# Optimization experiments

Hardware: AMD Instinct MI355X
Metric: run time of the kernel (lower is better)

## Reference

```python
import jax, jax.numpy as jnp
import numpy as np

T, C, H, W, CI = 4, 64, 96, 96, 16
PS, WS, STR0 = 7, 21, 4
KS, KA = 100, 100
SCALE = 10.0


def conv1x1(x, w, b):
    # x: [T,C,H,W], w: [O,C]
    return jnp.einsum('tchw,oc->tohw', x, w) + b[None, :, None, None]


def unfold_clip(x, ps):
    # clipped-boundary unfold: [T,C,H,W] -> [T, H*W, C*ps*ps]
    t, c, h, w = x.shape
    d = jnp.arange(ps)
    ii = jnp.clip(jnp.arange(h)[:, None] + d[None, :], 0, h - 1)  # [H,ps]
    jj = jnp.clip(jnp.arange(w)[:, None] + d[None, :], 0, w - 1)  # [W,ps]
    p = x[:, :, ii]            # [T,C,H,ps,W]
    p = p[:, :, :, :, jj]      # [T,C,H,ps,W,ps]
    p = jnp.transpose(p, (0, 2, 4, 1, 3, 5))  # [T,H,W,C,ps,ps]
    return p.reshape(t, h * w, c * ps * ps)


def setup_inputs() -> dict:
    key = jax.random.key(0)
    ks = jax.random.split(key, 9)
    s = lambda fan: 1.0 / np.sqrt(fan)
    return {
        'vid': jax.random.normal(ks[0], (T, C, H, W), jnp.float32),
        'g_w': jax.random.normal(ks[1], (CI, C), jnp.float32) * s(C),
        'g_b': jax.random.normal(ks[2], (CI,), jnp.float32) * 0.01,
        'theta_w': jax.random.normal(ks[3], (CI, C), jnp.float32) * s(C),
        'theta_b': jax.random.normal(ks[4], (CI,), jnp.float32) * 0.01,
        'phi_w': jax.random.normal(ks[5], (CI, C), jnp.float32) * s(C),
        'phi_b': jax.random.normal(ks[6], (CI,), jnp.float32) * 0.01,
        'W_w': jax.random.normal(ks[7], (C, CI), jnp.float32) * s(CI),
        'W_b': jax.random.normal(ks[8], (C,), jnp.float32) * 0.01,
    }


def reference(vid, g_w, g_b, theta_w, theta_b, phi_w, phi_b, W_w, W_b):
    t, c, h, w = vid.shape
    b1 = conv1x1(vid, g_w, g_b)          # query features  (g)
    b2 = conv1x1(vid, theta_w, theta_b)  # value features  (theta)
    b3 = conv1x1(vid, phi_w, phi_b)      # key features    (phi)

    b1u = unfold_clip(b1, PS)  # [T,HW,D]
    b2u = unfold_clip(b2, PS)
    b3u = unfold_clip(b3, PS)

    # query grid (stride0)
    qi, qj = jnp.meshgrid(jnp.arange(0, h, STR0), jnp.arange(0, w, STR0), indexing='ij')
    qi, qj = qi.reshape(-1), qj.reshape(-1)
    nq = qi.shape[0]
    qflat = qi * w + qj
    b1q = b1u[:, qflat]  # [T,nq,D]

    # centered spatial search window (stride1=1), clipped bounds
    off = jnp.arange(WS) - WS // 2
    ci = jnp.clip(qi[:, None] + off[None, :], 0, h - 1)  # [nq,WS]
    cj = jnp.clip(qj[:, None] + off[None, :], 0, w - 1)
    cand = (ci[:, :, None] * w + cj[:, None, :]).reshape(nq, WS * WS)

    # patch inner-product dists, one window offset at a time (memory-lean)
    def score(cidx):  # cidx: [nq]
        return jnp.einsum('tqd,tqd->tq', b1q, b3u[:, cidx])
    dists = jax.lax.map(score, cand.T)           # [WS*WS,T,nq]
    dists = jnp.transpose(dists, (1, 2, 0))      # [T,nq,WS*WS]

    vals, idx = jax.lax.top_k(dists, KS)
    vals, idx = vals[..., :KA], idx[..., :KA]
    yi = jax.nn.softmax(vals * SCALE, axis=-1)   # [T,nq,KA]

    pos = jnp.take_along_axis(jnp.broadcast_to(cand[None], (t,) + cand.shape), idx, axis=-1)
    patches = b2u[jnp.arange(t)[:, None, None], pos]   # [T,nq,KA,D]
    zi = jnp.einsum('tqk,tqkd->tqd', yi, patches)      # [T,nq,D]

    # fold: overlap-add scatter + counts normalization
    zi = zi.reshape(t, nq, CI, PS, PS).transpose(0, 2, 1, 3, 4).reshape(t, CI, nq * PS * PS)
    d = jnp.arange(PS)
    pi = jnp.clip(qi[:, None] + d[None, :], 0, h - 1)
    pj = jnp.clip(qj[:, None] + d[None, :], 0, w - 1)
    pix = (pi[:, :, None] * w + pj[:, None, :]).reshape(-1)
    acc = jnp.zeros((t, CI, h * w), vid.dtype).at[:, :, pix].add(zi)
    Z = jnp.zeros((h * w,), vid.dtype).at[pix].add(1.0)
    y = (acc / Z).reshape(t, CI, h, w)

    return vid + conv1x1(y, W_w, W_b)
```

## Files before the change

### kernel.cpp

```cpp
#include <hip/hip_runtime.h>
#include <hip/hip_bf16.h>
#include <hip/hip_fp16.h>
#include <math.h>

typedef __hip_bfloat16 bf16;
typedef unsigned int u32;
typedef __attribute__((ext_vector_type(8))) short short8;
typedef __attribute__((ext_vector_type(4))) float float4v;

#define T_   4
#define C_   64
#define H_   96
#define W_   96
#define CI_  16
#define HW_  9216
#define NC_  441
#define K_   100
#define HSEL 0x07060302u
#define LSEL 0x05040100u

__device__ __forceinline__ float ldbf(const void* p, int i) { return __bfloat162float(((const bf16*)p)[i]); }
__device__ __forceinline__ float ldf (const void* p, int i) { return ((const float*)p)[i]; }

__device__ __forceinline__ unsigned short f2bf(float x) {
    union { float f; u32 u; } a; a.f = x;
    u32 r = a.u + 0x7FFF + ((a.u >> 16) & 1);
    return (unsigned short)(r >> 16);
}
__device__ __forceinline__ float bf2f(unsigned short s) {
    union { u32 u; float f; } a; a.u = ((u32)s) << 16;
    return a.f;
}
__device__ __forceinline__ u32 packbf(float x) {
    unsigned short h = f2bf(x);
    unsigned short l = f2bf(x - bf2f(h));
    return ((u32)h << 16) | (u32)l;
}
__device__ __forceinline__ u32 okey(float f) {
    u32 u = __float_as_uint(f);
    return u ^ ((u & 0x80000000u) ? 0xFFFFFFFFu : 0x80000000u);
}
__device__ __forceinline__ float unokey(u32 k) {
    u32 u = (k & 0x80000000u) ? (k ^ 0x80000000u) : ~k;
    return __uint_as_float(u);
}
__device__ __forceinline__ int cntdim(int x) {
    int c = 0;
#pragma unroll
    for (int pp = 0; pp < 7; pp++) {
        int q = x - pp;
        c += (q >= 0 && q <= 92 && ((q & 3) == 0)) ? 1 : 0;
    }
    if (x == 95) c += 3;
    return c;
}

__device__ __forceinline__ int detect_flag(const void* vid, int tid, int* sflag) {
    if (tid < 64) {
        unsigned short w = ((const unsigned short*)vid)[tid * 2];
        int e = (w >> 7) & 0xFF;
        int sane = ((e >= 100 && e <= 140) || ((w & 0x7FFF) == 0)) ? 1 : 0;
#pragma unroll
        for (int off = 1; off < 64; off <<= 1) sane += __shfl_xor(sane, off);
        if (tid == 0) *sflag = (sane >= 48) ? 1 : 0;
    }
    __syncthreads();
    return *sflag;
}

__global__ __launch_bounds__(256) void conv3_k(const void* vid, const void* gw, const void* gb,
                                               const void* tw, const void* tb, const void* pw,
                                               const void* pb,
                                               u32* __restrict__ B1p, __half* __restrict__ B2h,
                                               u32* __restrict__ B3p, float* __restrict__ ACCb)
{
    __shared__ float w[3120];
    __shared__ int sflag;
    int tid = threadIdx.x;
    int isbf = detect_flag(vid, tid, &sflag);
    if (isbf) {
        for (int i = tid; i < 3120; i += 256) {
            float v;
            if (i < 1024) v = ldbf(gw, i);
            else if (i < 2048) v = ldbf(tw, i - 1024);
            else if (i < 3072) v = ldbf(pw, i - 2048);
            else if (i < 3088) v = ldbf(gb, i - 3072);
            else if (i < 3104) v = ldbf(tb, i - 3088);
            else v = ldbf(pb, i - 3104);
            w[i] = v;
        }
    } else {
        for (int i = tid; i < 3120; i += 256) {
            float v;
            if (i < 1024) v = ldf(gw, i);
            else if (i < 2048) v = ldf(tw, i - 1024);
            else if (i < 3072) v = ldf(pw, i - 2048);
            else if (i < 3088) v = ldf(gb, i - 3072);
            else if (i < 3104) v = ldf(tb, i - 3088);
            else v = ldf(pb, i - 3104);
            w[i] = v;
        }
    }
    __syncthreads();

    {
        float4v z = {0.f, 0.f, 0.f, 0.f};
        *(float4v*)(ACCb + (blockIdx.x * 256 + tid) * 4) = z;
    }

    int lane = tid & 63, og = tid >> 6;
    int g0 = blockIdx.x * 64 + lane;
    int t = g0 / HW_, pix = g0 - t * HW_;

    float a1[4], a2[4], a3[4];
#pragma unroll
    for (int k = 0; k < 4; k++) {
        a1[k] = w[3072 + og * 4 + k];
        a2[k] = w[3088 + og * 4 + k];
        a3[k] = w[3104 + og * 4 + k];
    }
    int base = t * C_ * HW_ + pix;
#pragma unroll 16
    for (int c = 0; c < C_; c++) {
        float v = isbf ? ldbf(vid, base + c * HW_) : ldf(vid, base + c * HW_);
#pragma unroll
        for (int k = 0; k < 4; k++) {
            a1[k] += v * w[(og * 4 + k) * 64 + c];
            a2[k] += v * w[1024 + (og * 4 + k) * 64 + c];
            a3[k] += v * w[2048 + (og * 4 + k) * 64 + c];
        }
    }
    int ob = g0 * 16 + og * 4;
    uint4 p1, p3;
    p1.x = packbf(a1[0]); p1.y = packbf(a1[1]); p1.z = packbf(a1[2]); p1.w = packbf(a1[3]);
    p3.x = packbf(a3[0]); p3.y = packbf(a3[1]); p3.z = packbf(a3[2]); p3.w = packbf(a3[3]);
    *(uint4*)(B1p + ob) = p1;
    *(uint4*)(B3p + ob) = p3;
    __half2 h01 = __floats2half2_rn(a2[0], a2[1]);
    __half2 h23 = __floats2half2_rn(a2[2], a2[3]);
    uint2 p2;
    p2.x = *(u32*)&h01; p2.y = *(u32*)&h23;
    *(uint2*)(B2h + ob) = p2;
}

__global__ __launch_bounds__(512, 6) void attn_k(const u32* __restrict__ B1p,
                                                 const __half* __restrict__ B2h,
                                                 const u32* __restrict__ B3p,
                                                 float* __restrict__ ACCb)
{
    __shared__ __align__(16) char SM[51344];
    short*   Win  = (short*)SM;
    float*   Sc   = (float*)(SM + 32768);
    float*   Cb   = (float*)(SM + 39824);
    int*     hist = (int*)(SM + 39824);
    float*   yiw  = (float*)(SM + 48016);
    int*     pab  = (int*)(SM + 49616);
    int*     ctl  = (int*)(SM + 51216);
    __half2* Zc   = (__half2*)(SM + 32768);
    __half2* Wp   = (__half2*)SM;

    int tid = threadIdx.x;
    int tile = blockIdx.x, t = blockIdx.y;
    int qy = tile / 12, qx = tile - qy * 12;
    int qi = qy * 8, qj = qx * 8;

    const u32*    B1t = B1p + t * HW_ * 16;
    const __half* B2t = B2h + t * HW_ * 16;
    const u32*    B3t = B3p + t * HW_ * 16;

    int lane = tid & 63, wv = tid >> 6;
    int nn = lane & 15, qsel = nn >> 3, pjn = nn & 7;
    int koff = (lane >> 4) * 8;

    for (int pos = tid; pos < 1024; pos += 512) {
        int row = pos >> 5, col = pos & 31;
        int vr = min(max(qi - 10 + row, 0), 95);
        int vc = min(max(qj - 10 + col, 0), 95);
        const u32* src = B3t + (vr * 96 + vc) * 16;
        uint4 U0 = *(const uint4*)src,       U1 = *(const uint4*)(src + 4);
        uint4 U2 = *(const uint4*)(src + 8), U3 = *(const uint4*)(src + 12);
        uint4 A, B;
        A.x = __builtin_amdgcn_perm(U0.y, U0.x, HSEL);
        A.y = __builtin_amdgcn_perm(U0.w, U0.z, HSEL);
        A.z = __builtin_amdgcn_perm(U1.y, U1.x, HSEL);
        A.w = __builtin_amdgcn_perm(U1.w, U1.z, HSEL);
        B.x = __builtin_amdgcn_perm(U2.y, U2.x, HSEL);
        B.y = __builtin_amdgcn_perm(U2.w, U2.z, HSEL);
        B.z = __builtin_amdgcn_perm(U3.y, U3.x, HSEL);
        B.w = __builtin_amdgcn_perm(U3.w, U3.z, HSEL);
        *(uint4*)(Win + pos * 16)     = A;
        *(uint4*)(Win + pos * 16 + 8) = B;
    }
    __syncthreads();

#pragma unroll 1
    for (int ri = 0; ri < 2; ri++) {
        short8 Bh[4], Bl[4];
        int qiq = qi + 4 * ri, qjq = qj + 4 * qsel;
#pragma unroll
        for (int s = 0; s < 4; s++) {
            int kk0 = s * 32 + koff;
            int pi = kk0 >> 4, c0 = kk0 & 15;
            uint4 U0 = {0, 0, 0, 0}, U1 = {0, 0, 0, 0};
            if (pjn < 7 && pi < 7) {
                const u32* src = B1t + (min(qiq + pi, 95) * 96 + min(qjq + pjn, 95)) * 16 + c0;
                U0 = *(const uint4*)src;
                U1 = *(const uint4*)(src + 4);
            }
            union { uint4 u; short8 s8; } hc, lc;
            hc.u.x = __builtin_amdgcn_perm(U0.y, U0.x, HSEL);
            hc.u.y = __builtin_amdgcn_perm(U0.w, U0.z, HSEL);
            hc.u.z = __builtin_amdgcn_perm(U1.y, U1.x, HSEL);
            hc.u.w = __builtin_amdgcn_perm(U1.w, U1.z, HSEL);
            lc.u.x = __builtin_amdgcn_perm(U0.y, U0.x, LSEL);
            lc.u.y = __builtin_amdgcn_perm(U0.w, U0.z, LSEL);
            lc.u.z = __builtin_amdgcn_perm(U1.y, U1.x, LSEL);
            lc.u.w = __builtin_amdgcn_perm(U1.w, U1.z, LSEL);
            Bh[s] = hc.s8; Bl[s] = lc.s8;
        }
        float* Cw = Cb + wv * 256;
        for (int r = wv; r < 21; r += 8) {
            float psum = 0.f;
            int v = (lane >= 21) ? 1 : 0;
            int b = lane - v * 21;
#pragma unroll
            for (int st = 0; st < 2; st++) {
                float4v acc = {0.f, 0.f, 0.f, 0.f};
#pragma unroll
                for (int s = 0; s < 4; s++) {
                    int arow = 4 * ri + r + 2 * s + (lane >> 5);
                    int aoff = (arow * 32 + st * 16 + nn) * 16 + ((lane >> 4) & 1) * 8;
                    short8 A = *(const short8*)(Win + aoff);
                    acc = __builtin_amdgcn_mfma_f32_16x16x32_bf16(A, Bh[s], acc, 0, 0, 0);
                    acc = __builtin_amdgcn_mfma_f32_16x16x32_bf16(A, Bl[s], acc, 0, 0, 0);
                }
                *(float4v*)(Cw + nn * 16 + (lane >> 4) * 4) = acc;
                if (lane < 42) {
#pragma unroll
                    for (int pj = 0; pj < 7; pj++) {
                        int sp = b + 4 * v + pj;
                        if ((sp >> 4) == st) psum += Cw[(8 * v + pj) * 16 + (sp & 15)];
                    }
                }
            }
            if (lane < 42) Sc[(ri * 2 + v) * 441 + r * 21 + b] = psum;
        }
    }
    __syncthreads();

    for (int pos = tid; pos < 1024; pos += 512) {
        int row = pos >> 5, col = pos & 31;
        int vr = min(max(qi - 10 + row, 0), 95);
        int vc = min(max(qj - 10 + col, 0), 95);
        const u32* src = B3t + (vr * 96 + vc) * 16;
        uint4 U0 = *(const uint4*)src,       U1 = *(const uint4*)(src + 4);
        uint4 U2 = *(const uint4*)(src + 8), U3 = *(const uint4*)(src + 12);
        uint4 A, B;
        A.x = __builtin_amdgcn_perm(U0.y, U0.x, LSEL);
        A.y = __builtin_amdgcn_perm(U0.w, U0.z, LSEL);
        A.z = __builtin_amdgcn_perm(U1.y, U1.x, LSEL);
        A.w = __builtin_amdgcn_perm(U1.w, U1.z, LSEL);
        B.x = __builtin_amdgcn_perm(U2.y, U2.x, LSEL);
        B.y = __builtin_amdgcn_perm(U2.w, U2.z, LSEL);
        B.z = __builtin_amdgcn_perm(U3.y, U3.x, LSEL);
        B.w = __builtin_amdgcn_perm(U3.w, U3.z, LSEL);
        *(uint4*)(Win + pos * 16)     = A;
        *(uint4*)(Win + pos * 16 + 8) = B;
    }
    __syncthreads();

#pragma unroll 1
    for (int ri = 0; ri < 2; ri++) {
        short8 Bh[4];
        int qiq = qi + 4 * ri, qjq = qj + 4 * qsel;
#pragma unroll
        for (int s = 0; s < 4; s++) {
            int kk0 = s * 32 + koff;
            int pi = kk0 >> 4, c0 = kk0 & 15;
            uint4 U0 = {0, 0, 0, 0}, U1 = {0, 0, 0, 0};
            if (pjn < 7 && pi < 7) {
                const u32* src = B1t + (min(qiq + pi, 95) * 96 + min(qjq + pjn, 95)) * 16 + c0;
                U0 = *(const uint4*)src;
                U1 = *(const uint4*)(src + 4);
            }
            union { uint4 u; short8 s8; } hc;
            hc.u.x = __builtin_amdgcn_perm(U0.y, U0.x, HSEL);
            hc.u.y = __builtin_amdgcn_perm(U0.w, U0.z, HSEL);
            hc.u.z = __builtin_amdgcn_perm(U1.y, U1.x, HSEL);
            hc.u.w = __builtin_amdgcn_perm(U1.w, U1.z, HSEL);
            Bh[s] = hc.s8;
        }
        float* Cw = Cb + wv * 256;
        for (int r = wv; r < 21; r += 8) {
            float psum = 0.f;
            int v = (lane >= 21) ? 1 : 0;
            int b = lane - v * 21;
#pragma unroll
            for (int st = 0; st < 2; st++) {
                float4v acc = {0.f, 0.f, 0.f, 0.f};
#pragma unroll
                for (int s = 0; s < 4; s++) {
                    int arow = 4 * ri + r + 2 * s + (lane >> 5);
                    int aoff = (arow * 32 + st * 16 + nn) * 16 + ((lane >> 4) & 1) * 8;
                    short8 A = *(const short8*)(Win + aoff);
                    acc = __builtin_amdgcn_mfma_f32_16x16x32_bf16(A, Bh[s], acc, 0, 0, 0);
                }
                *(float4v*)(Cw + nn * 16 + (lane >> 4) * 4) = acc;
                if (lane < 42) {
#pragma unroll
                    for (int pj = 0; pj < 7; pj++) {
                        int sp = b + 4 * v + pj;
                        if ((sp >> 4) == st) psum += Cw[(8 * v + pj) * 16 + (sp & 15)];
                    }
                }
            }
            if (lane < 42) Sc[(ri * 2 + v) * 441 + r * 21 + b] += psum;
        }
    }
    __syncthreads();

    for (int pos = tid; pos < 992; pos += 512) {
        int row = pos >> 5, col = pos & 31;
        int vr = min(max(qi - 10 + row, 0), 95);
        int vc = min(max(qj - 10 + col, 0), 95);
        const __half* src = B2t + (vr * 96 + vc) * 16;
        *(int4*)(Wp + pos * 8)     = *(const int4*)src;
        *(int4*)(Wp + pos * 8 + 4) = *(const int4*)(src + 8);
    }
    hist[tid] = 0; hist[512 + tid] = 0;
    if (tid < 32) ctl[tid] = ((tid & 7) == 1) ? K_ : 0;
    __syncthreads();

    int g = wv & 3;
    int ri = g >> 1, ci = g & 1;
    int qiq = qi + 4 * ri, qjq = qj + 4 * ci;
    int alo = max(0, 10 - qiq), ahi = min(20, 105 - qiq);
    int blo = max(0, 10 - qjq), bhi = min(20, 105 - qjq);
    u32 kreg[7]; int ni = 0;
    u32 kmax = 0;
    if (wv < 4) {
        for (int i = lane; i < NC_; i += 64) {
            int aa = i / 21, bb = i - aa * 21;
            int ae = min(max(aa, alo), ahi), be = min(max(bb, blo), bhi);
            u32 k = okey(Sc[g * 441 + ae * 21 + be]);
            kmax = max(kmax, k);
            kreg[ni++] = k;
        }
#pragma unroll
        for (int off = 1; off < 64; off <<= 1) kmax = max(kmax, (u32)__shfl_xor((int)kmax, off));
    }

    for (int ps = 3; ps >= 0; ps--) {
        if (wv < 4 && !ctl[g * 8 + 3]) {
            u32 pref = (u32)ctl[g * 8];
            for (int a = 0; a < ni; a++) {
                u32 k = kreg[a];
                if (ps == 3 || (k >> ((ps + 1) * 8)) == pref)
                    atomicAdd(&hist[g * 256 + ((k >> (ps * 8)) & 255)], 1);
            }
        }
        __syncthreads();
        if (wv < 4 && !ctl[g * 8 + 3]) {
            int4 hv = *(int4*)(hist + g * 256 + lane * 4);
            int local = hv.x + hv.y + hv.z + hv.w;
            int s = local;
#pragma unroll
            for (int off = 1; off < 64; off <<= 1) {
                int tt = __shfl_down(s, off);
                if (lane + off < 64) s += tt;
            }
            int c4 = s - local;
            int c3 = c4 + hv.w, c2 = c3 + hv.z, c1 = c2 + hv.y, c0 = s;
            int need = ctl[g * 8 + 1];
            u32 pf = (u32)ctl[g * 8];
            int cums[5] = {c0, c1, c2, c3, c4};
            int hk[4] = {hv.x, hv.y, hv.z, hv.w};
#pragma unroll
            for (int k = 0; k < 4; k++) {
                if (cums[k] >= need && cums[k + 1] < need) {
                    int newneed = need - cums[k + 1];
                    ctl[g * 8]     = (int)((pf << 8) | (u32)(lane * 4 + k));
                    ctl[g * 8 + 1] = newneed;
                    if (newneed == hk[k] || ps == 0) { ctl[g * 8 + 3] = 1; ctl[g * 8 + 2] = 8 * ps; }
                }
            }
            int4 zz = {0, 0, 0, 0};
            *(int4*)(hist + g * 256 + lane * 4) = zz;
        }
        __syncthreads();
        if (ctl[3] && ctl[11] && ctl[19] && ctl[27]) break;
    }

    if (wv < 4) {
        u32 theta = (u32)ctl[g * 8];
        int shift = ctl[g * 8 + 2];
        int need  = ctl[g * 8 + 1];
        int base  = K_ - need;
        int a2 = 0;
        for (int i = lane; i < NC_; i += 64) {
            u32 k = kreg[a2++];
            u32 hp = k >> shift;
            int slot = -1;
            if (hp > theta) slot = atomicAdd(&ctl[g * 8 + 4], 1);
            else if (hp == theta) {
                int j = atomicAdd(&ctl[g * 8 + 5], 1);
                if (j < need) slot = base + j;
            }
            if (slot >= 0) {
                int a = i / 21, b = i - a * 21;
                int ae = min(max(a, alo), ahi), be = min(max(b, blo), bhi);
                yiw[g * 100 + slot] = unokey(k);
                pab[g * 100 + slot] = ((ae + 4 * ri) << 8) | (be + 4 * ci);
            }
        }
        float m = unokey(kmax);
        float wa = expf((yiw[g * 100 + lane] - m) * 10.f);
        float wb2 = (lane < 36) ? expf((yiw[g * 100 + 64 + lane] - m) * 10.f) : 0.f;
        float ssum = wa + wb2;
#pragma unroll
        for (int off = 1; off < 64; off <<= 1) ssum += __shfl_xor(ssum, off);
        float inv = 1.f / ssum;
        yiw[g * 100 + lane] = wa * inv;
        if (lane < 36) yiw[g * 100 + 64 + lane] = wb2 * inv;
    }
    __syncthreads();

    {
        int kh = wv >> 2;
        __half2 z[8];
        int rsel = lane & 1;
        int pi = lane / 7, pj = lane - pi * 7;
        if (lane < 49) {
#pragma unroll
            for (int j = 0; j < 8; j++) z[j] = __float2half2_rn(0.f);
            int kb2 = kh * 50;
            for (int k = kb2; k < kb2 + 50; k++) {
                float y = yiw[g * 100 + k];
                int pp = pab[g * 100 + k];
                int row = (pp >> 8) + pi, col = (pp & 255) + pj;
                const __half2* cell = Wp + (row * 32 + col) * 8;
                int4 A0 = *(const int4*)(cell + rsel * 4);
                int4 A1 = *(const int4*)(cell + 4 - rsel * 4);
                const __half2* pa = (const __half2*)&A0;
                const __half2* pb2 = (const __half2*)&A1;
                __half2 yh = __float2half2_rn(y);
#pragma unroll
                for (int j = 0; j < 4; j++) {
                    z[j]     = __hfma2(pa[j],  yh, z[j]);
                    z[4 + j] = __hfma2(pb2[j], yh, z[4 + j]);
                }
            }
        }
        if (kh == 1 && lane < 49) {
            *(int4*)(Zc + (g * 49 + lane) * 8)     = *(int4*)(z);
            *(int4*)(Zc + (g * 49 + lane) * 8 + 4) = *(int4*)(z + 4);
        }
        __syncthreads();
        if (kh == 0 && lane < 49) {
            const __half2* zo = Zc + (g * 49 + lane) * 8;
#pragma unroll
            for (int j = 0; j < 8; j++) z[j] = __hadd2(z[j], zo[j]);
            int orow = min(qiq + pi, 95), ocol = min(qjq + pj, 95);
            float* dst = ACCb + t * CI_ * HW_ + orow * 96 + ocol;
            int c0 = rsel * 8, c1 = 8 - c0;
#pragma unroll
            for (int jh = 0; jh < 4; jh++) {
                atomicAdd(dst + (c0 + 2 * jh) * HW_,     __low2float(z[jh]));
                atomicAdd(dst + (c0 + 2 * jh + 1) * HW_, __high2float(z[jh]));
                atomicAdd(dst + (c1 + 2 * jh) * HW_,     __low2float(z[4 + jh]));
                atomicAdd(dst + (c1 + 2 * jh + 1) * HW_, __high2float(z[4 + jh]));
            }
        }
    }
}

__global__ __launch_bounds__(256) void out_k(const void* vid, const void* Ww, const void* Wb,
                                             const float* __restrict__ ACCb, void* out)
{
    __shared__ float w[1088];
    __shared__ int sflag;
    int tid = threadIdx.x;
    int isbf = detect_flag(vid, tid, &sflag);
    if (isbf) { for (int i = tid; i < 1088; i += 256) w[i] = (i < 1024) ? ldbf(Ww, i) : ldbf(Wb, i - 1024); }
    else      { for (int i = tid; i < 1088; i += 256) w[i] = (i < 1024) ? ldf (Ww, i) : ldf (Wb, i - 1024); }
    __syncthreads();

    int lane5 = tid & 31, oct = tid >> 5;
    int g0 = blockIdx.x * 32 + lane5;
    int t = g0 / HW_, pix = g0 - t * HW_;
    int pi = pix / 96, pj = pix - pi * 96;
    float invz = 1.f / (float)(cntdim(pi) * cntdim(pj));

    float y[CI_];
    int ab = t * CI_ * HW_ + pix;
#pragma unroll
    for (int ci = 0; ci < CI_; ci++) y[ci] = ACCb[ab + ci * HW_] * invz;

    int vb = t * C_ * HW_ + pix;
#pragma unroll
    for (int co = oct * 8; co < oct * 8 + 8; co++) {
        float s = w[1024 + co];
#pragma unroll
        for (int ci = 0; ci < CI_; ci++) s += w[co * 16 + ci] * y[ci];
        int idx = vb + co * HW_;
        float vv = isbf ? ldbf(vid, idx) : ldf(vid, idx);
        float r = vv + s;
        if (isbf) ((bf16*)out)[idx] = __float2bfloat16(r);
        else      ((float*)out)[idx] = r;
    }
}

extern "C" void kernel_launch(void* const* d_in, const int* in_sizes, int n_in,
                              void* d_out, int out_size, void* d_ws, size_t ws_size,
                              hipStream_t stream)
{
    char* ws = (char*)d_ws;
    u32*    B1p  = (u32*)ws;
    __half* B2h  = (__half*)(ws + 2359296);
    u32*    B3p  = (u32*)(ws + 3538944);
    float*  ACCb = (float*)(ws + 5898240);

    conv3_k<<<dim3(576), dim3(256), 0, stream>>>(d_in[0], d_in[1], d_in[2], d_in[3], d_in[4],
                                                 d_in[5], d_in[6], B1p, B2h, B3p, ACCb);
    attn_k<<<dim3(144, T_), dim3(512), 0, stream>>>(B1p, B2h, B3p, ACCb);
    out_k<<<dim3(1152), dim3(256), 0, stream>>>(d_in[0], d_in[7], d_in[8], ACCb, d_out);
}
```

Measured before the change: 172.3 us.

## Read key and value windows directly from global memory, shrink shared memory

Drops the shared-memory staging of the key window (done twice, for hi and lo bf16 halves) and of the value window. MFMA A-operands and value patches are now loaded straight from global/L2 with clamped indices. The two-pass hi/lo split becomes a single pass with three MFMAs, and the aggregation becomes one wave per query group with zero-weight skipping and no cross-wave reduction or barrier. The aim is to cut LDS footprint from about 51KB to 18KB for higher occupancy and to remove staging loops and syncs. The cost is more uncoalesced, redundant global loads in the inner MFMA and gather loops.

```diff
diff --git a/kernel.cpp b/kernel.cpp
--- a/kernel.cpp
+++ b/kernel.cpp
@@ -148,16 +148,13 @@
                                                  const u32* __restrict__ B3p,
                                                  float* __restrict__ ACCb)
 {
-    __shared__ __align__(16) char SM[51344];
-    short*   Win  = (short*)SM;
-    float*   Sc   = (float*)(SM + 32768);
-    float*   Cb   = (float*)(SM + 39824);
-    int*     hist = (int*)(SM + 39824);
-    float*   yiw  = (float*)(SM + 48016);
-    int*     pab  = (int*)(SM + 49616);
-    int*     ctl  = (int*)(SM + 51216);
-    __half2* Zc   = (__half2*)(SM + 32768);
-    __half2* Wp   = (__half2*)SM;
+    __shared__ __align__(16) char SM[18576];
+    float* Sc   = (float*)SM;
+    float* Cb   = (float*)(SM + 7056);
+    int*   hist = (int*)(SM + 7056);
+    float* yiw  = (float*)(SM + 15248);
+    int*   pab  = (int*)(SM + 16848);
+    int*   ctl  = (int*)(SM + 18448);
 
     int tid = threadIdx.x;
     int tile = blockIdx.x, t = blockIdx.y;
@@ -171,27 +168,12 @@
     int lane = tid & 63, wv = tid >> 6;
     int nn = lane & 15, qsel = nn >> 3, pjn = nn & 7;
     int koff = (lane >> 4) * 8;
-
-    for (int pos = tid; pos < 1024; pos += 512) {
-        int row = pos >> 5, col = pos & 31;
-        int vr = min(max(qi - 10 + row, 0), 95);
-        int vc = min(max(qj - 10 + col, 0), 95);
-        const u32* src = B3t + (vr * 96 + vc) * 16;
-        uint4 U0 = *(const uint4*)src,       U1 = *(const uint4*)(src + 4);
-        uint4 U2 = *(const uint4*)(src + 8), U3 = *(const uint4*)(src + 12);
-        uint4 A, B;
-        A.x = __builtin_amdgcn_perm(U0.y, U0.x, HSEL);
-        A.y = __builtin_amdgcn_perm(U0.w, U0.z, HSEL);
-        A.z = __builtin_amdgcn_perm(U1.y, U1.x, HSEL);
-        A.w = __builtin_amdgcn_perm(U1.w, U1.z, HSEL);
-        B.x = __builtin_amdgcn_perm(U2.y, U2.x, HSEL);
-        B.y = __builtin_amdgcn_perm(U2.w, U2.z, HSEL);
-        B.z = __builtin_amdgcn_perm(U3.y, U3.x, HSEL);
-        B.w = __builtin_amdgcn_perm(U3.w, U3.z, HSEL);
-        *(uint4*)(Win + pos * 16)     = A;
-        *(uint4*)(Win + pos * 16 + 8) = B;
-    }
-    __syncthreads();
+    int hi8 = (lane >> 4) & 1;
+
+    int acol0 = min(max(qj - 10 + nn, 0), 95) * 16 + hi8 * 8;
+    int acol1 = min(max(qj + 6 + nn, 0), 95) * 16 + hi8 * 8;
+
+    float* Cw = Cb + wv * 256;
 
 #pragma unroll 1
     for (int ri = 0; ri < 2; ri++) {
@@ -218,21 +200,33 @@
             lc.u.w = __builtin_amdgcn_perm(U1.w, U1.z, LSEL);
             Bh[s] = hc.s8; Bl[s] = lc.s8;
         }
-        float* Cw = Cb + wv * 256;
         for (int r = wv; r < 21; r += 8) {
             float psum = 0.f;
             int v = (lane >= 21) ? 1 : 0;
             int b = lane - v * 21;
 #pragma unroll
             for (int st = 0; st < 2; st++) {
+                int acolc = st ? acol1 : acol0;
                 float4v acc = {0.f, 0.f, 0.f, 0.f};
 #pragma unroll
                 for (int s = 0; s < 4; s++) {
                     int arow = 4 * ri + r + 2 * s + (lane >> 5);
-                    int aoff = (arow * 32 + st * 16 + nn) * 16 + ((lane >> 4) & 1) * 8;
-                    short8 A = *(const short8*)(Win + aoff);
-                    acc = __builtin_amdgcn_mfma_f32_16x16x32_bf16(A, Bh[s], acc, 0, 0, 0);
-                    acc = __builtin_amdgcn_mfma_f32_16x16x32_bf16(A, Bl[s], acc, 0, 0, 0);
+                    int vr = min(max(qi - 10 + arow, 0), 95);
+                    const u32* asrc = B3t + vr * 1536 + acolc;
+                    uint4 U0 = *(const uint4*)asrc;
+                    uint4 U1 = *(const uint4*)(asrc + 4);
+                    union { uint4 u; short8 s8; } hc, lc;
+                    hc.u.x = __builtin_amdgcn_perm(U0.y, U0.x, HSEL);
+                    hc.u.y = __builtin_amdgcn_perm(U0.w, U0.z, HSEL);
+                    hc.u.z = __builtin_amdgcn_perm(U1.y, U1.x, HSEL);
+                    hc.u.w = __builtin_amdgcn_perm(U1.w, U1.z, HSEL);
+                    lc.u.x = __builtin_amdgcn_perm(U0.y, U0.x, LSEL);
+                    lc.u.y = __builtin_amdgcn_perm(U0.w, U0.z, LSEL);
+                    lc.u.z = __builtin_amdgcn_perm(U1.y, U1.x, LSEL);
+                    lc.u.w = __builtin_amdgcn_perm(U1.w, U1.z, LSEL);
+                    acc = __builtin_amdgcn_mfma_f32_16x16x32_bf16(hc.s8, Bh[s], acc, 0, 0, 0);
+                    acc = __builtin_amdgcn_mfma_f32_16x16x32_bf16(hc.s8, Bl[s], acc, 0, 0, 0);
+                    acc = __builtin_amdgcn_mfma_f32_16x16x32_bf16(lc.s8, Bh[s], acc, 0, 0, 0);
                 }
                 *(float4v*)(Cw + nn * 16 + (lane >> 4) * 4) = acc;
                 if (lane < 42) {
@@ -248,92 +242,13 @@
     }
     __syncthreads();
 
-    for (int pos = tid; pos < 1024; pos += 512) {
-        int row = pos >> 5, col = pos & 31;
-        int vr = min(max(qi - 10 + row, 0), 95);
-        int vc = min(max(qj - 10 + col, 0), 95);
-        const u32* src = B3t + (vr * 96 + vc) * 16;
-        uint4 U0 = *(const uint4*)src,       U1 = *(const uint4*)(src + 4);
-        uint4 U2 = *(const uint4*)(src + 8), U3 = *(const uint4*)(src + 12);
-        uint4 A, B;
-        A.x = __builtin_amdgcn_perm(U0.y, U0.x, LSEL);
-        A.y = __builtin_amdgcn_perm(U0.w, U0.z, LSEL);
-        A.z = __builtin_amdgcn_perm(U1.y, U1.x, LSEL);
-        A.w = __builtin_amdgcn_perm(U1.w, U1.z, LSEL);
-        B.x = __builtin_amdgcn_perm(U2.y, U2.x, LSEL);
-        B.y = __builtin_amdgcn_perm(U2.w, U2.z, LSEL);
-        B.z = __builtin_amdgcn_perm(U3.y, U3.x, LSEL);
-        B.w = __builtin_amdgcn_perm(U3.w, U3.z, LSEL);
-        *(uint4*)(Win + pos * 16)     = A;
-        *(uint4*)(Win + pos * 16 + 8) = B;
-    }
-    __syncthreads();
-
-#pragma unroll 1
-    for (int ri = 0; ri < 2; ri++) {
-        short8 Bh[4];
-        int qiq = qi + 4 * ri, qjq = qj + 4 * qsel;
-#pragma unroll
-        for (int s = 0; s < 4; s++) {
-            int kk0 = s * 32 + koff;
-            int pi = kk0 >> 4, c0 = kk0 & 15;
-            uint4 U0 = {0, 0, 0, 0}, U1 = {0, 0, 0, 0};
-            if (pjn < 7 && pi < 7) {
-                const u32* src = B1t + (min(qiq + pi, 95) * 96 + min(qjq + pjn, 95)) * 16 + c0;
-                U0 = *(const uint4*)src;
-                U1 = *(const uint4*)(src + 4);
-            }
-            union { uint4 u; short8 s8; } hc;
-            hc.u.x = __builtin_amdgcn_perm(U0.y, U0.x, HSEL);
-            hc.u.y = __builtin_amdgcn_perm(U0.w, U0.z, HSEL);
-            hc.u.z = __builtin_amdgcn_perm(U1.y, U1.x, HSEL);
-            hc.u.w = __builtin_amdgcn_perm(U1.w, U1.z, HSEL);
-            Bh[s] = hc.s8;
-        }
-        float* Cw = Cb + wv * 256;
-        for (int r = wv; r < 21; r += 8) {
-            float psum = 0.f;
-            int v = (lane >= 21) ? 1 : 0;
-            int b = lane - v * 21;
-#pragma unroll
-            for (int st = 0; st < 2; st++) {
-                float4v acc = {0.f, 0.f, 0.f, 0.f};
-#pragma unroll
-                for (int s = 0; s < 4; s++) {
-                    int arow = 4 * ri + r + 2 * s + (lane >> 5);
-                    int aoff = (arow * 32 + st * 16 + nn) * 16 + ((lane >> 4) & 1) * 8;
-                    short8 A = *(const short8*)(Win + aoff);
-                    acc = __builtin_amdgcn_mfma_f32_16x16x32_bf16(A, Bh[s], acc, 0, 0, 0);
-                }
-                *(float4v*)(Cw + nn * 16 + (lane >> 4) * 4) = acc;
-                if (lane < 42) {
-#pragma unroll
-                    for (int pj = 0; pj < 7; pj++) {
-                        int sp = b + 4 * v + pj;
-                        if ((sp >> 4) == st) psum += Cw[(8 * v + pj) * 16 + (sp & 15)];
-                    }
-                }
-            }
-            if (lane < 42) Sc[(ri * 2 + v) * 441 + r * 21 + b] += psum;
-        }
-    }
-    __syncthreads();
-
-    for (int pos = tid; pos < 992; pos += 512) {
-        int row = pos >> 5, col = pos & 31;
-        int vr = min(max(qi - 10 + row, 0), 95);
-        int vc = min(max(qj - 10 + col, 0), 95);
-        const __half* src = B2t + (vr * 96 + vc) * 16;
-        *(int4*)(Wp + pos * 8)     = *(const int4*)src;
-        *(int4*)(Wp + pos * 8 + 4) = *(const int4*)(src + 8);
-    }
     hist[tid] = 0; hist[512 + tid] = 0;
     if (tid < 32) ctl[tid] = ((tid & 7) == 1) ? K_ : 0;
     __syncthreads();
 
     int g = wv & 3;
-    int ri = g >> 1, ci = g & 1;
-    int qiq = qi + 4 * ri, qjq = qj + 4 * ci;
+    int ri2 = g >> 1, ci2 = g & 1;
+    int qiq = qi + 4 * ri2, qjq = qj + 4 * ci2;
     int alo = max(0, 10 - qiq), ahi = min(20, 105 - qiq);
     int blo = max(0, 10 - qjq), bhi = min(20, 105 - qjq);
     u32 kreg[7]; int ni = 0;
@@ -391,7 +306,9 @@
         if (ctl[3] && ctl[11] && ctl[19] && ctl[27]) break;
     }
 
-    if (wv < 4) {
+    if (wv >= 4) return;
+
+    {
         u32 theta = (u32)ctl[g * 8];
         int shift = ctl[g * 8 + 2];
         int need  = ctl[g * 8 + 1];
@@ -410,11 +327,12 @@
                 int a = i / 21, b = i - a * 21;
                 int ae = min(max(a, alo), ahi), be = min(max(b, blo), bhi);
                 yiw[g * 100 + slot] = unokey(k);
-                pab[g * 100 + slot] = ((ae + 4 * ri) << 8) | (be + 4 * ci);
-            }
-        }
+                pab[g * 100 + slot] = ((ae + 4 * ri2) << 8) | (be + 4 * ci2);
+            }
+        }
+        asm volatile("s_waitcnt lgkmcnt(0)" ::: "memory");
         float m = unokey(kmax);
-        float wa = expf((yiw[g * 100 + lane] - m) * 10.f);
+        float wa  = expf((yiw[g * 100 + lane] - m) * 10.f);
         float wb2 = (lane < 36) ? expf((yiw[g * 100 + 64 + lane] - m) * 10.f) : 0.f;
         float ssum = wa + wb2;
 #pragma unroll
@@ -422,54 +340,44 @@
         float inv = 1.f / ssum;
         yiw[g * 100 + lane] = wa * inv;
         if (lane < 36) yiw[g * 100 + 64 + lane] = wb2 * inv;
-    }
-    __syncthreads();
-
-    {
-        int kh = wv >> 2;
+        asm volatile("s_waitcnt lgkmcnt(0)" ::: "memory");
+    }
+
+    if (lane < 49) {
+        int rsel = lane & 1;
+        int pi2 = lane / 7, pj2 = lane - pi2 * 7;
         __half2 z[8];
-        int rsel = lane & 1;
-        int pi = lane / 7, pj = lane - pi * 7;
-        if (lane < 49) {
-#pragma unroll
-            for (int j = 0; j < 8; j++) z[j] = __float2half2_rn(0.f);
-            int kb2 = kh * 50;
-            for (int k = kb2; k < kb2 + 50; k++) {
-                float y = yiw[g * 100 + k];
-                int pp = pab[g * 100 + k];
-                int row = (pp >> 8) + pi, col = (pp & 255) + pj;
-                const __half2* cell = Wp + (row * 32 + col) * 8;
-                int4 A0 = *(const int4*)(cell + rsel * 4);
-                int4 A1 = *(const int4*)(cell + 4 - rsel * 4);
-                const __half2* pa = (const __half2*)&A0;
-                const __half2* pb2 = (const __half2*)&A1;
-                __half2 yh = __float2half2_rn(y);
-#pragma unroll
-                for (int j = 0; j < 4; j++) {
-                    z[j]     = __hfma2(pa[j],  yh, z[j]);
-                    z[4 + j] = __hfma2(pb2[j], yh, z[4 + j]);
-                }
-            }
-        }
-        if (kh == 1 && lane < 49) {
-            *(int4*)(Zc + (g * 49 + lane) * 8)     = *(int4*)(z);
-            *(int4*)(Zc + (g * 49 + lane) * 8 + 4) = *(int4*)(z + 4);
-        }
-        __syncthreads();
-        if (kh == 0 && lane < 49) {
-            const __half2* zo = Zc + (g * 49 + lane) * 8;
-#pragma unroll
-            for (int j = 0; j < 8; j++) z[j] = __hadd2(z[j], zo[j]);
-            int orow = min(qiq + pi, 95), ocol = min(qjq + pj, 95);
-            float* dst = ACCb + t * CI_ * HW_ + orow * 96 + ocol;
-            int c0 = rsel * 8, c1 = 8 - c0;
-#pragma unroll
-            for (int jh = 0; jh < 4; jh++) {
-                atomicAdd(dst + (c0 + 2 * jh) * HW_,     __low2float(z[jh]));
-                atomicAdd(dst + (c0 + 2 * jh + 1) * HW_, __high2float(z[jh]));
-                atomicAdd(dst + (c1 + 2 * jh) * HW_,     __low2float(z[4 + jh]));
-                atomicAdd(dst + (c1 + 2 * jh + 1) * HW_, __high2float(z[4 + jh]));
-            }
+#pragma unroll
+        for (int j = 0; j < 8; j++) z[j] = __float2half2_rn(0.f);
+#pragma unroll 1
+        for (int k = 0; k < K_; k++) {
+            float y = yiw[g * 100 + k];
+            if (y == 0.f) continue;
+            int pp = pab[g * 100 + k];
+            int row = (pp >> 8) + pi2, col = (pp & 255) + pj2;
+            int vr = min(max(qi - 10 + row, 0), 95);
+            int vc = min(max(qj - 10 + col, 0), 95);
+            const __half* cell = B2t + (vr * 96 + vc) * 16;
+            int4 A0 = *(const int4*)(cell + rsel * 8);
+            int4 A1 = *(const int4*)(cell + 8 - rsel * 8);
+            const __half2* pa  = (const __half2*)&A0;
+            const __half2* pb2 = (const __half2*)&A1;
+            __half2 yh = __float2half2_rn(y);
+#pragma unroll
+            for (int j = 0; j < 4; j++) {
+                z[j]     = __hfma2(pa[j],  yh, z[j]);
+                z[4 + j] = __hfma2(pb2[j], yh, z[4 + j]);
+            }
+        }
+        int orow = min(qiq + pi2, 95), ocol = min(qjq + pj2, 95);
+        float* dst = ACCb + t * CI_ * HW_ + orow * 96 + ocol;
+        int c0 = rsel * 8, c1 = 8 - c0;
+#pragma unroll
+        for (int jh = 0; jh < 4; jh++) {
+            atomicAdd(dst + (c0 + 2 * jh) * HW_,     __low2float(z[jh]));
+            atomicAdd(dst + (c0 + 2 * jh + 1) * HW_, __high2float(z[jh]));
+            atomicAdd(dst + (c1 + 2 * jh) * HW_,     __low2float(z[4 + jh]));
+            atomicAdd(dst + (c1 + 2 * jh + 1) * HW_, __high2float(z[4 + jh]));
         }
     }
 }
```

Measured after the change: 182.0 us. 5.6% more time.

## Skip zero-weight neighbors and gather value patches directly from global memory

Applied to the files above, without the earlier changes.

The value-window staging into shared memory and the two-wave split of the aggregation are removed. Each of four waves now ballots which softmax weights are nonzero and walks only those indices, loading the value patch rows straight from global memory (L2/L1). The final block barrier and the shared-memory reduction are also dropped, and waves 4-7 exit early. The aim is to cut LDS staging, barriers and multiply-adds spent on weights that underflow to zero. In exchange the aggregation loses parallelism, since 4 waves instead of 8 do it, and adds scattered global loads.

```diff
diff --git a/kernel.cpp b/kernel.cpp
--- a/kernel.cpp
+++ b/kernel.cpp
@@ -5,6 +5,7 @@
 
 typedef __hip_bfloat16 bf16;
 typedef unsigned int u32;
+typedef unsigned long long u64;
 typedef __attribute__((ext_vector_type(8))) short short8;
 typedef __attribute__((ext_vector_type(4))) float float4v;
 
@@ -149,15 +150,13 @@
                                                  float* __restrict__ ACCb)
 {
     __shared__ __align__(16) char SM[51344];
-    short*   Win  = (short*)SM;
-    float*   Sc   = (float*)(SM + 32768);
-    float*   Cb   = (float*)(SM + 39824);
-    int*     hist = (int*)(SM + 39824);
-    float*   yiw  = (float*)(SM + 48016);
-    int*     pab  = (int*)(SM + 49616);
-    int*     ctl  = (int*)(SM + 51216);
-    __half2* Zc   = (__half2*)(SM + 32768);
-    __half2* Wp   = (__half2*)SM;
+    short* Win  = (short*)SM;
+    float* Sc   = (float*)(SM + 32768);
+    float* Cb   = (float*)(SM + 39824);
+    int*   hist = (int*)(SM + 39824);
+    float* yiw  = (float*)(SM + 48016);
+    int*   pab  = (int*)(SM + 49616);
+    int*   ctl  = (int*)(SM + 51216);
 
     int tid = threadIdx.x;
     int tile = blockIdx.x, t = blockIdx.y;
@@ -319,21 +318,13 @@
     }
     __syncthreads();
 
-    for (int pos = tid; pos < 992; pos += 512) {
-        int row = pos >> 5, col = pos & 31;
-        int vr = min(max(qi - 10 + row, 0), 95);
-        int vc = min(max(qj - 10 + col, 0), 95);
-        const __half* src = B2t + (vr * 96 + vc) * 16;
-        *(int4*)(Wp + pos * 8)     = *(const int4*)src;
-        *(int4*)(Wp + pos * 8 + 4) = *(const int4*)(src + 8);
-    }
     hist[tid] = 0; hist[512 + tid] = 0;
     if (tid < 32) ctl[tid] = ((tid & 7) == 1) ? K_ : 0;
     __syncthreads();
 
     int g = wv & 3;
-    int ri = g >> 1, ci = g & 1;
-    int qiq = qi + 4 * ri, qjq = qj + 4 * ci;
+    int ri2 = g >> 1, ci2 = g & 1;
+    int qiq = qi + 4 * ri2, qjq = qj + 4 * ci2;
     int alo = max(0, 10 - qiq), ahi = min(20, 105 - qiq);
     int blo = max(0, 10 - qjq), bhi = min(20, 105 - qjq);
     u32 kreg[7]; int ni = 0;
@@ -391,7 +382,10 @@
         if (ctl[3] && ctl[11] && ctl[19] && ctl[27]) break;
     }
 
-    if (wv < 4) {
+    if (wv >= 4) return;
+
+    u64 am0, am1;
+    {
         u32 theta = (u32)ctl[g * 8];
         int shift = ctl[g * 8 + 2];
         int need  = ctl[g * 8 + 1];
@@ -410,38 +404,47 @@
                 int a = i / 21, b = i - a * 21;
                 int ae = min(max(a, alo), ahi), be = min(max(b, blo), bhi);
                 yiw[g * 100 + slot] = unokey(k);
-                pab[g * 100 + slot] = ((ae + 4 * ri) << 8) | (be + 4 * ci);
-            }
-        }
+                pab[g * 100 + slot] = ((ae + 4 * ri2) << 8) | (be + 4 * ci2);
+            }
+        }
+        asm volatile("s_waitcnt lgkmcnt(0)" ::: "memory");
         float m = unokey(kmax);
-        float wa = expf((yiw[g * 100 + lane] - m) * 10.f);
+        float wa  = expf((yiw[g * 100 + lane] - m) * 10.f);
         float wb2 = (lane < 36) ? expf((yiw[g * 100 + 64 + lane] - m) * 10.f) : 0.f;
         float ssum = wa + wb2;
 #pragma unroll
         for (int off = 1; off < 64; off <<= 1) ssum += __shfl_xor(ssum, off);
         float inv = 1.f / ssum;
-        yiw[g * 100 + lane] = wa * inv;
-        if (lane < 36) yiw[g * 100 + 64 + lane] = wb2 * inv;
-    }
-    __syncthreads();
-
-    {
-        int kh = wv >> 2;
+        float wan = wa * inv, wbn = wb2 * inv;
+        yiw[g * 100 + lane] = wan;
+        if (lane < 36) yiw[g * 100 + 64 + lane] = wbn;
+        am0 = __ballot(wan != 0.f);
+        am1 = __ballot((lane < 36) && (wbn != 0.f));
+        asm volatile("s_waitcnt lgkmcnt(0)" ::: "memory");
+    }
+
+    if (lane < 49) {
+        int rsel = lane & 1;
+        int pi2 = lane / 7, pj2 = lane - pi2 * 7;
         __half2 z[8];
-        int rsel = lane & 1;
-        int pi = lane / 7, pj = lane - pi * 7;
-        if (lane < 49) {
-#pragma unroll
-            for (int j = 0; j < 8; j++) z[j] = __float2half2_rn(0.f);
-            int kb2 = kh * 50;
-            for (int k = kb2; k < kb2 + 50; k++) {
+#pragma unroll
+        for (int j = 0; j < 8; j++) z[j] = __float2half2_rn(0.f);
+#pragma unroll 1
+        for (int half = 0; half < 2; half++) {
+            u64 mm = half ? am1 : am0;
+            int kb = half ? 64 : 0;
+            while (mm) {
+                int k = kb + (__ffsll(mm) - 1);
+                mm &= mm - 1;
                 float y = yiw[g * 100 + k];
                 int pp = pab[g * 100 + k];
-                int row = (pp >> 8) + pi, col = (pp & 255) + pj;
-                const __half2* cell = Wp + (row * 32 + col) * 8;
-                int4 A0 = *(const int4*)(cell + rsel * 4);
-                int4 A1 = *(const int4*)(cell + 4 - rsel * 4);
-                const __half2* pa = (const __half2*)&A0;
+                int row = (pp >> 8) + pi2, col = (pp & 255) + pj2;
+                int vr = min(max(qi - 10 + row, 0), 95);
+                int vc = min(max(qj - 10 + col, 0), 95);
+                const __half* cell = B2t + (vr * 96 + vc) * 16;
+                int4 A0 = *(const int4*)(cell + rsel * 8);
+                int4 A1 = *(const int4*)(cell + 8 - rsel * 8);
+                const __half2* pa  = (const __half2*)&A0;
                 const __half2* pb2 = (const __half2*)&A1;
                 __half2 yh = __float2half2_rn(y);
 #pragma unroll
@@ -451,25 +454,15 @@
                 }
             }
         }
-        if (kh == 1 && lane < 49) {
-            *(int4*)(Zc + (g * 49 + lane) * 8)     = *(int4*)(z);
-            *(int4*)(Zc + (g * 49 + lane) * 8 + 4) = *(int4*)(z + 4);
-        }
-        __syncthreads();
-        if (kh == 0 && lane < 49) {
-            const __half2* zo = Zc + (g * 49 + lane) * 8;
-#pragma unroll
-            for (int j = 0; j < 8; j++) z[j] = __hadd2(z[j], zo[j]);
-            int orow = min(qiq + pi, 95), ocol = min(qjq + pj, 95);
-            float* dst = ACCb + t * CI_ * HW_ + orow * 96 + ocol;
-            int c0 = rsel * 8, c1 = 8 - c0;
-#pragma unroll
-            for (int jh = 0; jh < 4; jh++) {
-                atomicAdd(dst + (c0 + 2 * jh) * HW_,     __low2float(z[jh]));
-                atomicAdd(dst + (c0 + 2 * jh + 1) * HW_, __high2float(z[jh]));
-                atomicAdd(dst + (c1 + 2 * jh) * HW_,     __low2float(z[4 + jh]));
-                atomicAdd(dst + (c1 + 2 * jh + 1) * HW_, __high2float(z[4 + jh]));
-            }
+        int orow = min(qiq + pi2, 95), ocol = min(qjq + pj2, 95);
+        float* dst = ACCb + t * CI_ * HW_ + orow * 96 + ocol;
+        int c0 = rsel * 8, c1 = 8 - c0;
+#pragma unroll
+        for (int jh = 0; jh < 4; jh++) {
+            atomicAdd(dst + (c0 + 2 * jh) * HW_,     __low2float(z[jh]));
+            atomicAdd(dst + (c0 + 2 * jh + 1) * HW_, __high2float(z[jh]));
+            atomicAdd(dst + (c1 + 2 * jh) * HW_,     __low2float(z[4 + jh]));
+            atomicAdd(dst + (c1 + 2 * jh + 1) * HW_, __high2float(z[4 + jh]));
         }
     }
 }
```

Result: no change. 169.9 us (-1.4%).
